# Kernel tuning notes

Measured on AMD Instinct MI355X. Metric: run time of the kernel, lower is better.

Reference implementation:

```python
import jax, jax.numpy as jnp
import numpy as np

B, K, D, V = 8192, 32, 128, 2048
WEIGHT, SIGMA, NDCG_K = 0.15, 1.0, 10
N = K + 1


def _to_hyperboloid(x):
    # lift spatial coords onto Lorentz hyperboloid: x0 = sqrt(1 + ||x||^2)
    t = jnp.sqrt(1.0 + jnp.sum(x * x, axis=-1, keepdims=True))
    return jnp.concatenate([t, x], axis=-1)


def _lorentz_dist(u, v):
    # d(u,v) = arccosh(-<u,v>_L), <u,v>_L = -u0*v0 + u[1:].v[1:]
    inner = -u[..., 0] * v[..., 0] + jnp.sum(u[..., 1:] * v[..., 1:], axis=-1)
    return jnp.arccosh(jnp.maximum(-inner, 1.0 + 1e-7))


def setup_inputs() -> dict:
    key = jax.random.key(0)
    k = jax.random.split(key, 7)
    anchor_emb = _to_hyperboloid(jax.random.normal(k[0], (B, D), dtype=jnp.float32))
    positive_emb = _to_hyperboloid(jax.random.normal(k[1], (B, D), dtype=jnp.float32))
    negative_embs = _to_hyperboloid(jax.random.normal(k[2], (B * K, D), dtype=jnp.float32))
    tree_distances = jax.random.uniform(k[3], (V, V), dtype=jnp.float32) * 10.0
    anchor_idx = jax.random.randint(k[4], (B,), 0, V, dtype=jnp.int32)
    pos_idx = jax.random.randint(k[5], (B,), 0, V, dtype=jnp.int32)
    neg_idx = jax.random.randint(k[6], (B, K), 0, V, dtype=jnp.int32)
    return {"anchor_emb": anchor_emb, "positive_emb": positive_emb,
            "negative_embs": negative_embs, "tree_distances": tree_distances,
            "anchor_idx": anchor_idx, "pos_idx": pos_idx, "neg_idx": neg_idx}


def _lambdarank(anchor_emb, positive_emb, negative_embs, tree_distances,
                anchor_idx, pos_idx, neg_idx):
    neg = negative_embs.reshape(B, K, -1)
    pos_dist = _lorentz_dist(anchor_emb, positive_emb)            # (B,)
    neg_dists = _lorentz_dist(anchor_emb[:, None, :], neg)        # (B,K)
    d = jnp.concatenate([pos_dist[:, None], neg_dists], axis=1)   # (B,N)

    pos_t = tree_distances[anchor_idx, pos_idx]                   # (B,)
    neg_t = tree_distances[anchor_idx[:, None], neg_idx]          # (B,K)
    t = jnp.concatenate([pos_t[:, None], neg_t], axis=1)          # (B,N)
    max_t = jnp.max(t, axis=1, keepdims=True)
    rel = (max_t - t + 1e-6) / (max_t + 1e-6)                     # (B,N)

    k_top = min(NDCG_K, N)
    # 1-based rank of each item under ascending-distance sort (piecewise const)
    ranks = jnp.argsort(jnp.argsort(d, axis=1), axis=1) + 1       # (B,N)
    disc = jnp.where(ranks <= k_top,
                     1.0 / jnp.log2(ranks.astype(jnp.float32) + 1.0), 0.0)
    ideal = -jnp.sort(-rel, axis=1)[:, :k_top]                    # (B,k)
    log_pos = jnp.log2(jnp.arange(2, k_top + 2, dtype=jnp.float32))
    idcg = jnp.sum(ideal / log_pos, axis=1)                       # (B,)

    # closed-form |delta NDCG| of swapping items i,j in the ranking:
    # |(rel_i - rel_j) * (disc_i - disc_j)| / IDCG
    drel = rel[:, :, None] - rel[:, None, :]                      # (B,N,N)
    ddisc = disc[:, :, None] - disc[:, None, :]
    inv_idcg = jnp.where(idcg > 0, 1.0 / idcg, 0.0)[:, None, None]
    delta = jnp.abs(drel * ddisc) * inv_idcg

    # lambda_ij = sign(rel_i-rel_j) * delta * sigmoid(sign * sigma * (d_j - d_i))
    S = jnp.sign(drel)
    dd = d[:, None, :] - d[:, :, None]                            # d_j - d_i
    lam = S * delta * jax.nn.sigmoid(S * SIGMA * dd)
    # loss = sum_{i<j} lam_ij*(d_i-d_j); antisymmetric -> 0.5 * full sum
    loss_b = 0.5 * jnp.sum(lam * (-dd), axis=(1, 2))              # (B,)
    return WEIGHT * jnp.mean(loss_b)


def reference(anchor_emb, positive_emb, negative_embs, tree_distances,
              anchor_idx, pos_idx, neg_idx):
    return _lambdarank(anchor_emb, positive_emb, negative_embs, tree_distances,
                       anchor_idx, pos_idx, neg_idx)
```

## Files before the change

kernel.cpp:

```cpp
#include <hip/hip_runtime.h>
#include <math.h>

#define BB 8192
#define KK 32
#define DD 129
#define VV 2048
#define NN 33
#define TOPK 10
#define WPB 4

__device__ __forceinline__ float fast_rcp(float x) { return __builtin_amdgcn_rcpf(x); }

__global__ __launch_bounds__(256) void lr_fused(
    const float* __restrict__ anchor,
    const float* __restrict__ positive,
    const float* __restrict__ neg,
    const float* __restrict__ tree,
    const int* __restrict__ a_idx,
    const int* __restrict__ p_idx,
    const int* __restrict__ n_idx,
    float* __restrict__ partial)
{
    __shared__ float  st_[WPB][NN];
    __shared__ float  sd_[WPB][NN];
    __shared__ float4 sitem[WPB][NN];

    const int t    = threadIdx.x;
    const int wave = t >> 6;
    const int lane = t & 63;
    const int g    = lane >> 4;
    const int subl = lane & 15;
    const int b    = blockIdx.x * WPB + wave;

    const int ai  = a_idx[b];
    const int col = (lane == 0) ? p_idx[b]
                                : n_idx[(size_t)b * KK + ((lane < NN ? lane : KK) - 1)];
    const float tg = tree[(size_t)ai * VV + col];

    const float* ab = anchor   + (size_t)b * DD;
    const float* pb = positive + (size_t)b * DD;
    const float* nb = neg      + (size_t)b * (KK * DD);

    float areg[8];
    #pragma unroll
    for (int e = 0; e < 8; ++e) areg[e] = ab[e * 16 + subl];
    const float a128 = ab[128];

    const float* rp[9];
    #pragma unroll
    for (int r = 0; r < 9; ++r) {
        int row = 4 * r + g;
        if (row > KK) row = KK;
        rp[r] = (row == 0) ? pb : (nb + (size_t)(row - 1) * DD);
    }
    float vv[9][8];
    #pragma unroll
    for (int r = 0; r < 9; ++r)
        #pragma unroll
        for (int e = 0; e < 8; ++e)
            vv[r][e] = rp[r][e * 16 + subl];
    float t128[9];
    #pragma unroll
    for (int r = 0; r < 9; ++r) t128[r] = rp[r][128];

    if (lane < NN) st_[wave][lane] = tg;

    #pragma unroll
    for (int r = 0; r < 9; ++r) {
        float s = 0.0f;
        #pragma unroll
        for (int e = 0; e < 8; ++e) s = fmaf(areg[e], vv[r][e], s);
        s += __shfl_xor(s, 8, 64);
        s += __shfl_xor(s, 4, 64);
        s += __shfl_xor(s, 2, 64);
        s += __shfl_xor(s, 1, 64);
        int row = 4 * r + g;
        if (subl == 0 && row < NN) {
            float full = s + a128 * t128[r];
            float x = fmaxf(fmaf(2.0f * areg[0], vv[r][0], -full), 1.0f + 1e-07f);
            sd_[wave][row] = __logf(x + sqrtf(x * x - 1.0f));
        }
    }
    __syncthreads();

    if (lane < NN) {
        float maxt = st_[wave][0];
        #pragma unroll
        for (int j = 1; j < NN; ++j) maxt = fmaxf(maxt, st_[wave][j]);
        float rel = (maxt - st_[wave][lane] + 1e-06f) * fast_rcp(maxt + 1e-06f);

        float di = sd_[wave][lane];
        int cnt = 0;
        #pragma unroll
        for (int j = 0; j < NN; ++j) {
            float dj = sd_[wave][j];
            cnt += (int)((dj < di) | ((dj == di) & (j < lane)));
        }
        float disc = (cnt + 1 <= TOPK) ? fast_rcp(log2f((float)(cnt + 2))) : 0.0f;
        sitem[wave][lane] = make_float4(di, rel, disc, 0.0f);
    }
    __syncthreads();

    float c = 0.0f;
    if (lane < NN) {
        float ri = sitem[wave][lane].y;
        int pos = 0;
        #pragma unroll
        for (int j = 0; j < NN; ++j) {
            float rj = sitem[wave][j].y;
            pos += (int)((rj > ri) | ((rj == ri) & (j < lane)));
        }
        if (pos < TOPK) c = ri * fast_rcp(log2f((float)(pos + 2)));
    }
    #pragma unroll
    for (int off = 32; off > 0; off >>= 1) c += __shfl_xor(c, off, 64);
    const float inv = (c > 0.0f) ? fast_rcp(c) : 0.0f;

    float acc = 0.0f;
    #pragma unroll
    for (int it = 0; it < 17; ++it) {
        int p = it * 64 + lane;
        int i = p / NN;
        int j = p - i * NN;
        float4 Ii = sitem[wave][i];
        float4 Ij = sitem[wave][j];
        float dd    = Ij.x - Ii.x;
        float drel  = Ii.y - Ij.y;
        float ddisc = Ii.z - Ij.z;
        float t1  = drel * fabsf(ddisc) * inv;
        float e   = __expf(-dd);
        float num = (drel >= 0.0f) ? 1.0f : e;
        acc = fmaf(t1 * num * fast_rcp(1.0f + e), -dd, acc);
    }
    #pragma unroll
    for (int off = 32; off > 0; off >>= 1) acc += __shfl_xor(acc, off, 64);
    if (lane == 0) partial[b] = 0.5f * acc;
}

__global__ __launch_bounds__(256) void lr_reduce(
    const float* __restrict__ partial, float* __restrict__ out)
{
    __shared__ float swave[4];
    const float4* p4 = (const float4*)partial;
    float acc = 0.0f;
    #pragma unroll
    for (int c = 0; c < (BB / 4) / 256; ++c) {
        float4 v = p4[c * 256 + threadIdx.x];
        acc += (v.x + v.y) + (v.z + v.w);
    }
    #pragma unroll
    for (int off = 32; off > 0; off >>= 1) acc += __shfl_xor(acc, off, 64);
    if ((threadIdx.x & 63) == 0) swave[threadIdx.x >> 6] = acc;
    __syncthreads();
    if (threadIdx.x == 0)
        out[0] = (swave[0] + swave[1] + swave[2] + swave[3]) * (0.15f / (float)BB);
}

extern "C" void kernel_launch(void* const* d_in, const int* in_sizes, int n_in,
                              void* d_out, int out_size, void* d_ws, size_t ws_size,
                              hipStream_t stream)
{
    const float* anchor   = (const float*)d_in[0];
    const float* positive = (const float*)d_in[1];
    const float* neg      = (const float*)d_in[2];
    const float* tree     = (const float*)d_in[3];
    const int*   a_idx    = (const int*)d_in[4];
    const int*   p_idx    = (const int*)d_in[5];
    const int*   n_idx    = (const int*)d_in[6];
    float* partial = (float*)d_ws;

    lr_fused<<<BB / WPB, 256, 0, stream>>>(anchor, positive, neg, tree,
                                           a_idx, p_idx, n_idx, partial);
    lr_reduce<<<1, 256, 0, stream>>>(partial, (float*)d_out);
}
```

Baseline: 224.5 us.

## Use pair symmetry to halve pair loop and drop block barriers

The pairwise lambda loop now runs over the 528 unordered pairs i<j, decoded with a triangular-index sqrt formula. Each pair contributes its full term, so the 0.5 factor is dropped. The two __syncthreads are removed, which is valid because each wave only touches its own LDS slice. The arccosh is also computed in parallel by lanes 0-32 rather than by the subl==0 lanes, and the tree-distance store moves earlier. The risks are float rounding in the sqrt-based index decode and reliance on wave-level ordering of LDS accesses without an explicit barrier.

New measurement: 222.2 us. Within noise of the previous version (-1.0%).

```diff
diff --git a/kernel.cpp b/kernel.cpp
--- a/kernel.cpp
+++ b/kernel.cpp
@@ -22,6 +22,7 @@
     float* __restrict__ partial)
 {
     __shared__ float  st_[WPB][NN];
+    __shared__ float  sx_[WPB][NN];
     __shared__ float  sd_[WPB][NN];
     __shared__ float4 sitem[WPB][NN];
 
@@ -36,6 +37,7 @@
     const int col = (lane == 0) ? p_idx[b]
                                 : n_idx[(size_t)b * KK + ((lane < NN ? lane : KK) - 1)];
     const float tg = tree[(size_t)ai * VV + col];
+    if (lane < NN) st_[wave][lane] = tg;
 
     const float* ab = anchor   + (size_t)b * DD;
     const float* pb = positive + (size_t)b * DD;
@@ -54,16 +56,13 @@
         rp[r] = (row == 0) ? pb : (nb + (size_t)(row - 1) * DD);
     }
     float vv[9][8];
-    #pragma unroll
-    for (int r = 0; r < 9; ++r)
-        #pragma unroll
-        for (int e = 0; e < 8; ++e)
-            vv[r][e] = rp[r][e * 16 + subl];
     float t128[9];
     #pragma unroll
-    for (int r = 0; r < 9; ++r) t128[r] = rp[r][128];
-
-    if (lane < NN) st_[wave][lane] = tg;
+    for (int r = 0; r < 9; ++r) {
+        #pragma unroll
+        for (int e = 0; e < 8; ++e) vv[r][e] = rp[r][e * 16 + subl];
+        t128[r] = rp[r][128];
+    }
 
     #pragma unroll
     for (int r = 0; r < 9; ++r) {
@@ -77,29 +76,32 @@
         int row = 4 * r + g;
         if (subl == 0 && row < NN) {
             float full = s + a128 * t128[r];
-            float x = fmaxf(fmaf(2.0f * areg[0], vv[r][0], -full), 1.0f + 1e-07f);
-            sd_[wave][row] = __logf(x + sqrtf(x * x - 1.0f));
+            sx_[wave][row] = fmaxf(fmaf(2.0f * areg[0], vv[r][0], -full), 1.0f + 1e-07f);
         }
     }
-    __syncthreads();
+
+    float dlane = 0.0f;
+    if (lane < NN) {
+        float x = sx_[wave][lane];
+        dlane = __logf(x + sqrtf(x * x - 1.0f));
+        sd_[wave][lane] = dlane;
+    }
 
     if (lane < NN) {
         float maxt = st_[wave][0];
         #pragma unroll
         for (int j = 1; j < NN; ++j) maxt = fmaxf(maxt, st_[wave][j]);
-        float rel = (maxt - st_[wave][lane] + 1e-06f) * fast_rcp(maxt + 1e-06f);
+        float rel = (maxt - tg + 1e-06f) * fast_rcp(maxt + 1e-06f);
 
-        float di = sd_[wave][lane];
         int cnt = 0;
         #pragma unroll
         for (int j = 0; j < NN; ++j) {
             float dj = sd_[wave][j];
-            cnt += (int)((dj < di) | ((dj == di) & (j < lane)));
+            cnt += (int)((dj < dlane) | ((dj == dlane) & (j < lane)));
         }
         float disc = (cnt + 1 <= TOPK) ? fast_rcp(log2f((float)(cnt + 2))) : 0.0f;
-        sitem[wave][lane] = make_float4(di, rel, disc, 0.0f);
+        sitem[wave][lane] = make_float4(dlane, rel, disc, 0.0f);
     }
-    __syncthreads();
 
     float c = 0.0f;
     if (lane < NN) {
@@ -118,23 +120,27 @@
 
     float acc = 0.0f;
     #pragma unroll
-    for (int it = 0; it < 17; ++it) {
+    for (int it = 0; it < 9; ++it) {
         int p = it * 64 + lane;
-        int i = p / NN;
-        int j = p - i * NN;
+        float vmask = (p < 528) ? 1.0f : 0.0f;
+        int pc = (p < 528) ? p : 527;
+        int j = (int)((1.0f + sqrtf((float)(8 * pc + 1))) * 0.5f);
+        int tj = (j * (j - 1)) >> 1;
+        if (tj > pc) { --j; tj = (j * (j - 1)) >> 1; }
+        int i = pc - tj;
         float4 Ii = sitem[wave][i];
         float4 Ij = sitem[wave][j];
         float dd    = Ij.x - Ii.x;
         float drel  = Ii.y - Ij.y;
         float ddisc = Ii.z - Ij.z;
-        float t1  = drel * fabsf(ddisc) * inv;
+        float t1  = drel * fabsf(ddisc) * (inv * vmask);
         float e   = __expf(-dd);
         float num = (drel >= 0.0f) ? 1.0f : e;
         acc = fmaf(t1 * num * fast_rcp(1.0f + e), -dd, acc);
     }
     #pragma unroll
     for (int off = 32; off > 0; off >>= 1) acc += __shfl_xor(acc, off, 64);
-    if (lane == 0) partial[b] = 0.5f * acc;
+    if (lane == 0) partial[b] = acc;
 }
 
 __global__ __launch_bounds__(256) void lr_reduce(
```
